# Kernel tuning notes

Hardware: AMD Instinct MI355X
Metric: run time of the kernel (lower is better)

The kernel has to match this reference:

```python
import jax, jax.numpy as jnp
import numpy as np


def setup_inputs() -> dict:
    key = jax.random.key(0)
    k1, k2 = jax.random.split(key)
    B, H, W, C = 16, 512, 512, 16
    moving_image = jax.random.normal(k1, (B, H, W, C), dtype=jnp.float32)
    deformation_matrix = jax.random.normal(k2, (B, H, W, 2), dtype=jnp.float32)
    return {"moving_image": moving_image, "deformation_matrix": deformation_matrix}


def reference(moving_image, deformation_matrix):
    # moving_image: [B, H, W, C] (channels-last), deformation_matrix: [B, H, W, 2]
    B, H, W, C = moving_image.shape
    # meshgrid of absolute pixel coordinates
    x_mesh = jnp.arange(W, dtype=moving_image.dtype)[None, None, :]   # [1,1,W]
    y_mesh = jnp.arange(H, dtype=moving_image.dtype)[None, :, None]   # [1,H,1]
    x = deformation_matrix[..., 0] + x_mesh                           # [B,H,W]
    y = deformation_matrix[..., 1] + y_mesh                           # [B,H,W]
    # zero-pad spatial dims by 1 (as F.pad(im, (0,0,1,1,1,1,0,0)))
    im = jnp.pad(moving_image, ((0, 0), (1, 1), (1, 1), (0, 0)))      # [B,H+2,W+2,C]
    Hp, Wp = H + 2, W + 2
    # shift coords into padded frame
    x = x + 1.0
    y = y + 1.0
    x0 = jnp.floor(x).astype(jnp.int32)
    y0 = jnp.floor(y).astype(jnp.int32)
    x1 = jnp.clip(x0 + 1, 0, Wp - 1)
    y1 = jnp.clip(y0 + 1, 0, Hp - 1)
    x0 = jnp.clip(x0, 0, Wp - 1)
    y0 = jnp.clip(y0, 0, Hp - 1)
    b = jnp.arange(B)[:, None, None]  # [B,1,1] broadcast batch index
    Ia = im[b, y0, x0]  # [B,H,W,C] top-left
    Ib = im[b, y1, x0]  # bottom-left
    Ic = im[b, y0, x1]  # top-right
    Id = im[b, y1, x1]  # bottom-right
    dx = x1.astype(x.dtype) - x
    dy = y1.astype(y.dtype) - y
    wa = (dx * dy)[..., None]
    wb = (dx * (1.0 - dy))[..., None]
    wc = ((1.0 - dx) * dy)[..., None]
    wd = ((1.0 - dx) * (1.0 - dy))[..., None]
    return wa * Ia + wb * Ib + wc * Ic + wd * Id
```

## Files before the change

kernel.cpp:

```cpp
#include <hip/hip_runtime.h>


#define H_ 512
#define W_ 512

typedef float v2f __attribute__((ext_vector_type(2)));
typedef float v4f __attribute__((ext_vector_type(4)));

__device__ __forceinline__ v4f bilerp_quad(const float* __restrict__ base,
                                           int cq, int xw, int y, v2f d)
{
    float xf = d.x + (float)xw + 1.0f;
    float yf = d.y + (float)y  + 1.0f;

    int x0 = (int)floorf(xf);
    int y0 = (int)floorf(yf);
    int x1 = min(max(x0 + 1, 0), W_ + 1);
    int y1 = min(max(y0 + 1, 0), H_ + 1);
    x0 = min(max(x0, 0), W_ + 1);
    y0 = min(max(y0, 0), H_ + 1);

    float dx = (float)x1 - xf;
    float dy = (float)y1 - yf;

    float vx0 = (x0 >= 1 && x0 <= W_) ? 1.0f : 0.0f;
    float vx1 = (x1 >= 1 && x1 <= W_) ? 1.0f : 0.0f;
    float vy0 = (y0 >= 1 && y0 <= H_) ? 1.0f : 0.0f;
    float vy1 = (y1 >= 1 && y1 <= H_) ? 1.0f : 0.0f;

    int xc0 = min(max(x0, 1), W_) - 1;
    int xc1 = min(max(x1, 1), W_) - 1;
    int yc0 = min(max(y0, 1), H_) - 1;
    int yc1 = min(max(y1, 1), H_) - 1;

    const float* pa = base + ((size_t)((yc0 << 9) | xc0) << 4) + cq;
    const float* pb = base + ((size_t)((yc1 << 9) | xc0) << 4) + cq;
    const float* pc = base + ((size_t)((yc0 << 9) | xc1) << 4) + cq;
    const float* pd = base + ((size_t)((yc1 << 9) | xc1) << 4) + cq;

    v4f Ia = *reinterpret_cast<const v4f*>(pa);
    v4f Ib = *reinterpret_cast<const v4f*>(pb);
    v4f Ic = *reinterpret_cast<const v4f*>(pc);
    v4f Id = *reinterpret_cast<const v4f*>(pd);

    float wa = dx * dy                   * (vx0 * vy0);
    float wb = dx * (1.0f - dy)          * (vx0 * vy1);
    float wc = (1.0f - dx) * dy          * (vx1 * vy0);
    float wd = (1.0f - dx) * (1.0f - dy) * (vx1 * vy1);

    return wa * Ia + wb * Ib + wc * Ic + wd * Id;
}

__global__ __launch_bounds__(256) void st_bilinear2(
    const float* __restrict__ img,
    const float* __restrict__ def,
    float* __restrict__ out)
{
    int tid = blockIdx.x * 256 + threadIdx.x;
    int cq  = (tid & 3) << 2;
    int pp  = tid >> 2;
    int xw  = pp & 511;
    int yh  = (pp >> 9) & 255;
    int b   = pp >> 17;
    int y0r = yh << 1;
    int p0  = (b << 18) | (y0r << 9) | xw;
    int p1  = p0 + W_;

    const float* base = img + ((size_t)b << 22);

    v2f d0 = __builtin_nontemporal_load(
        reinterpret_cast<const v2f*>(def + ((size_t)p0 << 1)));
    v2f d1 = __builtin_nontemporal_load(
        reinterpret_cast<const v2f*>(def + ((size_t)p1 << 1)));

    v4f r0 = bilerp_quad(base, cq, xw, y0r,     d0);
    v4f r1 = bilerp_quad(base, cq, xw, y0r + 1, d1);

    __builtin_nontemporal_store(r0, reinterpret_cast<v4f*>(out + ((size_t)p0 << 4) + cq));
    __builtin_nontemporal_store(r1, reinterpret_cast<v4f*>(out + ((size_t)p1 << 4) + cq));
}

extern "C" void kernel_launch(void* const* d_in, const int* in_sizes, int n_in,
                              void* d_out, int out_size, void* d_ws, size_t ws_size,
                              hipStream_t stream) {
    const float* img = (const float*)d_in[0];
    const float* def = (const float*)d_in[1];
    float* out = (float*)d_out;

    const int total_threads = 16 * 512 * 512 * 4 / 2;
    const int block = 256;
    const int grid = total_threads / block;

    st_bilinear2<<<grid, block, 0, stream>>>(img, def, out);
}
```

Measured before the change: 94.73 us.

## Process four rows per thread and swizzle block order across XCDs

Each thread now computes four consecutive rows for its pixel column and channel quad instead of two, which halves the thread count and grid size. Block indices are remapped so that consecutive hardware block IDs go to different slices of the work, aiming for better L2 locality per XCD given round-robin dispatch on MI355X. The intent is to amortize index math and improve gather-load reuse across adjacent rows. The cost is more registers per thread and fewer waves to hide memory latency.

```diff
diff --git a/kernel.cpp b/kernel.cpp
--- a/kernel.cpp
+++ b/kernel.cpp
@@ -51,33 +51,41 @@
     return wa * Ia + wb * Ib + wc * Ic + wd * Id;
 }
 
-__global__ __launch_bounds__(256) void st_bilinear2(
+__global__ __launch_bounds__(256) void st_bilinear4(
     const float* __restrict__ img,
     const float* __restrict__ def,
     float* __restrict__ out)
 {
-    int tid = blockIdx.x * 256 + threadIdx.x;
-    int cq  = (tid & 3) << 2;
-    int pp  = tid >> 2;
-    int xw  = pp & 511;
-    int yh  = (pp >> 9) & 255;
-    int b   = pp >> 17;
-    int y0r = yh << 1;
-    int p0  = (b << 18) | (y0r << 9) | xw;
-    int p1  = p0 + W_;
+    int sbid = (blockIdx.x & 7) * (16384 >> 3) + (blockIdx.x >> 3);
+    int tid  = sbid * 256 + threadIdx.x;
+
+    int cq   = (tid & 3) << 2;
+    int unit = tid >> 2;
+    int xw   = unit & 511;
+    int yg   = (unit >> 9) & 127;
+    int b    = unit >> 16;
+    int yr   = yg << 2;
+
+    int p0 = (b << 18) | (yr << 9) | xw;
 
     const float* base = img + ((size_t)b << 22);
+    const float* dp   = def + ((size_t)p0 << 1);
 
-    v2f d0 = __builtin_nontemporal_load(
-        reinterpret_cast<const v2f*>(def + ((size_t)p0 << 1)));
-    v2f d1 = __builtin_nontemporal_load(
-        reinterpret_cast<const v2f*>(def + ((size_t)p1 << 1)));
+    v2f d0 = __builtin_nontemporal_load(reinterpret_cast<const v2f*>(dp));
+    v2f d1 = __builtin_nontemporal_load(reinterpret_cast<const v2f*>(dp + (W_ << 1)));
+    v2f d2 = __builtin_nontemporal_load(reinterpret_cast<const v2f*>(dp + (W_ << 2)));
+    v2f d3 = __builtin_nontemporal_load(reinterpret_cast<const v2f*>(dp + 3 * (W_ << 1)));
 
-    v4f r0 = bilerp_quad(base, cq, xw, y0r,     d0);
-    v4f r1 = bilerp_quad(base, cq, xw, y0r + 1, d1);
+    v4f r0 = bilerp_quad(base, cq, xw, yr,     d0);
+    v4f r1 = bilerp_quad(base, cq, xw, yr + 1, d1);
+    v4f r2 = bilerp_quad(base, cq, xw, yr + 2, d2);
+    v4f r3 = bilerp_quad(base, cq, xw, yr + 3, d3);
 
-    __builtin_nontemporal_store(r0, reinterpret_cast<v4f*>(out + ((size_t)p0 << 4) + cq));
-    __builtin_nontemporal_store(r1, reinterpret_cast<v4f*>(out + ((size_t)p1 << 4) + cq));
+    float* op = out + ((size_t)p0 << 4) + cq;
+    __builtin_nontemporal_store(r0, reinterpret_cast<v4f*>(op));
+    __builtin_nontemporal_store(r1, reinterpret_cast<v4f*>(op + (W_ << 4)));
+    __builtin_nontemporal_store(r2, reinterpret_cast<v4f*>(op + (W_ << 5)));
+    __builtin_nontemporal_store(r3, reinterpret_cast<v4f*>(op + 3 * (W_ << 4)));
 }
 
 extern "C" void kernel_launch(void* const* d_in, const int* in_sizes, int n_in,
@@ -87,9 +95,9 @@
     const float* def = (const float*)d_in[1];
     float* out = (float*)d_out;
 
-    const int total_threads = 16 * 512 * 512 * 4 / 2;
+    const int total_threads = 16 * 512 * 512 * 4 / 4;
     const int block = 256;
     const int grid = total_threads / block;
 
-    st_bilinear2<<<grid, block, 0, stream>>>(img, def, out);
+    st_bilinear4<<<grid, block, 0, stream>>>(img, def, out);
 }
```

Result: slower. 123.0 us (+29.8%).
